# Kernel tuning notes

Hardware: AMD Instinct MI355X
Metric: run time of the kernel (lower is better)

Reference implementation:

```python
import jax, jax.numpy as jnp
import numpy as np

B = 256          # batch_size (number of graphs)
N = 512          # padded nodes per graph
IN_FEATS = 74
DIM = 128
E = 1_048_576    # total edges in batched graph
N_NODES = B * N


def setup_inputs() -> dict:
    key = jax.random.key(0)
    ks = jax.random.split(key, 10)
    x = jax.random.normal(ks[0], (N_NODES, IN_FEATS), dtype=jnp.float32)
    src = jax.random.randint(ks[1], (E,), 0, N_NODES, dtype=jnp.int32)
    dst = jax.random.randint(ks[2], (E,), 0, N_NODES, dtype=jnp.int32)
    # init_transform: Linear(in_feats, dim_embedding, bias=False); padding=True
    # zeroes weight[-1] (last OUTPUT row) -> last column in [in, out] layout.
    W_init = jax.random.normal(ks[3], (IN_FEATS, DIM), dtype=jnp.float32) * 0.1
    W_init = W_init.at[:, -1].set(0.0)
    W1 = jax.random.normal(ks[4], (DIM, DIM), dtype=jnp.float32) * 0.1
    W2 = jax.random.normal(ks[5], (DIM, DIM), dtype=jnp.float32) * 0.1
    W3 = jax.random.normal(ks[6], (DIM, DIM), dtype=jnp.float32) * 0.1
    b1 = jnp.zeros((DIM,), dtype=jnp.float32)
    b2 = jnp.zeros((DIM,), dtype=jnp.float32)
    b3 = jnp.zeros((DIM,), dtype=jnp.float32)
    return {"x": x, "src": src, "dst": dst, "W_init": W_init,
            "W1": W1, "b1": b1, "W2": W2, "b2": b2, "W3": W3, "b3": b3}


def _gcn_forward(x, src, dst, W_init, Ws, bs):
    n = x.shape[0]
    h = x @ W_init                                    # [n, DIM] initial embedding
    ones = jnp.ones(src.shape[0], dtype=x.dtype)
    deg_out = jax.ops.segment_sum(ones, src, num_segments=n)
    deg_in = jax.ops.segment_sum(ones, dst, num_segments=n)
    nrm_src = jax.lax.rsqrt(jnp.clip(deg_out, 1.0))   # D_out^{-1/2}
    nrm_dst = jax.lax.rsqrt(jnp.clip(deg_in, 1.0))    # D_in^{-1/2}
    for W, b in zip(Ws, bs):
        m = (h * nrm_src[:, None])[src]               # gather normalized messages [E, DIM]
        agg = jax.ops.segment_sum(m, dst, num_segments=n)  # scatter-add to dst nodes
        h = jax.nn.relu((agg * nrm_dst[:, None]) @ W + b)
    return h.reshape(B, N, -1)                        # [B, N, output_feats]


def reference(x, src, dst, W_init, W1, b1, W2, b2, W3, b3):
    return _gcn_forward(x, src, dst, W_init, (W1, W2, W3), (b1, b2, b3))
```

## Files before the change

kernel.cpp:

```cpp
#include <hip/hip_runtime.h>

#define NN 131072
#define NE 1048576
#define OFF_DEG_OUT 0x000000
#define OFF_CURSOR  0x080000
#define OFF_WT      0x100000
#define OFF_WTI     0x118000
#define OFF_BUCKET  0x200000
#define OFF_HN      0x2200000

typedef __attribute__((ext_vector_type(8))) short bf16x8;
typedef __attribute__((ext_vector_type(4))) float f32x4;

static __device__ __forceinline__ float blo(unsigned u){ return __uint_as_float(u << 16); }
static __device__ __forceinline__ float bhi(unsigned u){ return __uint_as_float(u & 0xffff0000u); }
static __device__ __forceinline__ unsigned f2b(float f){
    unsigned u = __float_as_uint(f);
    return (u + 0x7fffu + ((u >> 16) & 1u)) >> 16;
}
static __device__ __forceinline__ unsigned pack2(float a, float b){
    return f2b(a) | (f2b(b) << 16);
}

__global__ __launch_bounds__(256) void k_fill(const int* __restrict__ src,
                                              const int* __restrict__ dst,
                                              int* __restrict__ deg_out,
                                              int* __restrict__ cursor,
                                              int* __restrict__ bucket) {
    int base = (blockIdx.x * 256 + threadIdx.x) * 2;
    int2 s2 = *(const int2*)&src[base];
    int2 d2 = *(const int2*)&dst[base];
    int p0 = atomicAdd(&cursor[d2.x], 1);
    int p1 = atomicAdd(&cursor[d2.y], 1);
    atomicAdd(&deg_out[s2.x], 1);
    atomicAdd(&deg_out[s2.y], 1);
    if (p0 < 64) bucket[(size_t)d2.x * 64 + p0] = s2.x;
    if (p1 < 64) bucket[(size_t)d2.y * 64 + p1] = s2.y;
}

__global__ __launch_bounds__(256) void k_wprep(const float* __restrict__ W1,
                                               const float* __restrict__ W2,
                                               const float* __restrict__ W3,
                                               const float* __restrict__ Wi,
                                               unsigned short* __restrict__ Wt,
                                               unsigned short* __restrict__ Wti) {
    int idx = blockIdx.x * 256 + threadIdx.x;
    if (idx < 49152) {
        int L = idx >> 14, rem = idx & 16383;
        int k = rem >> 7, n = rem & 127;
        const float* W = L == 0 ? W1 : (L == 1 ? W2 : W3);
        Wt[L * 16384 + n * 128 + k] = (unsigned short)f2b(W[k * 128 + n]);
    } else if (idx < 61440) {
        int rem = idx - 49152;
        int n = rem / 96, k = rem - n * 96;
        float v = (k < 74) ? Wi[k * 128 + n] : 0.f;
        Wti[n * 96 + k] = (unsigned short)f2b(v);
    }
}

__global__ __launch_bounds__(256) void k_init(const float* __restrict__ X,
                                              const unsigned short* __restrict__ Wti,
                                              const int* __restrict__ deg_out,
                                              unsigned short* __restrict__ hn) {
    __shared__ unsigned int xs[64 * 68];
    int tid = threadIdx.x;
    int m0 = blockIdx.x * 64;

    for (int idx = tid; idx < 2368; idx += 256) {
        int m = idx / 37, t = idx - m * 37;
        float2 v = *(const float2*)&X[(size_t)(m0 + m) * 74 + t * 2];
        xs[m * 68 + t] = pack2(v.x, v.y);
    }
    for (int idx = tid; idx < 64 * 11; idx += 256) {
        int m = idx / 11, c = 37 + idx % 11;
        xs[m * 68 + c] = 0u;
    }
    __syncthreads();

    int wave = tid >> 6, lane = tid & 63, quad = lane >> 4, l16 = lane & 15;
    f32x4 acc[8];
    #pragma unroll
    for (int t = 0; t < 8; ++t) acc[t] = (f32x4){0.f, 0.f, 0.f, 0.f};
    int arow = (wave * 16 + l16) * 68 + quad * 4;
    #pragma unroll
    for (int ks = 0; ks < 3; ++ks) {
        bf16x8 af = *(const bf16x8*)&xs[arow + ks * 16];
        #pragma unroll
        for (int t = 0; t < 8; ++t) {
            bf16x8 bf = *(const bf16x8*)(Wti + (t * 16 + l16) * 96 + ks * 32 + quad * 8);
            acc[t] = __builtin_amdgcn_mfma_f32_16x16x32_bf16(af, bf, acc[t], 0, 0, 0);
        }
    }
    __syncthreads();
    unsigned short* atb = (unsigned short*)xs;
    int mb = wave * 16 + quad * 4;
    float nsr[4];
    #pragma unroll
    for (int r = 0; r < 4; ++r) {
        int dq = deg_out[m0 + mb + r];
        nsr[r] = rsqrtf((float)(dq > 1 ? dq : 1));
    }
    #pragma unroll
    for (int t = 0; t < 8; ++t)
        #pragma unroll
        for (int r = 0; r < 4; ++r)
            atb[(mb + r) * 136 + t * 16 + l16] = (unsigned short)f2b(acc[t][r] * nsr[r]);
    __syncthreads();
    {
        int r = tid >> 2, c0 = (tid & 3) * 32;
        unsigned int* sp = &xs[r * 68 + (tid & 3) * 16];
        #pragma unroll
        for (int j = 0; j < 4; ++j)
            *(uint4*)(hn + (size_t)(m0 + r) * 128 + c0 + j * 8) = *(const uint4*)(sp + j * 4);
    }
}

__global__ __launch_bounds__(256) void k_layer(const uint4* __restrict__ hn4,
                                               const int* __restrict__ bucket,
                                               const int* __restrict__ deg_in,
                                               const int* __restrict__ deg_out,
                                               const unsigned short* __restrict__ Wt,
                                               const float* __restrict__ bias,
                                               void* __restrict__ OutP, int last) {
    __shared__ unsigned int at[64 * 68];
    int tid = threadIdx.x;
    int m0 = blockIdx.x * 64;

    int g = tid >> 4, l16p = tid & 15;
    #pragma unroll
    for (int pass = 0; pass < 4; ++pass) {
        int nl = pass * 16 + g;
        int n = m0 + nl;
        int cnt = deg_in[n];
        cnt = cnt < 64 ? cnt : 64;
        const int* brow = bucket + (size_t)n * 64;
        float a0 = 0, a1 = 0, a2 = 0, a3 = 0, a4 = 0, a5 = 0, a6 = 0, a7 = 0;
        for (int c = 0; c < cnt; c += 8) {
            int4 sA = *(const int4*)&brow[c];
            int4 sB = *(const int4*)&brow[c + 4];
            int lim = cnt - c;
            int i1 = lim > 1 ? sA.y : 0;
            int i2 = lim > 2 ? sA.z : 0;
            int i3 = lim > 3 ? sA.w : 0;
            int i4 = lim > 4 ? sB.x : 0;
            int i5 = lim > 5 ? sB.y : 0;
            int i6 = lim > 6 ? sB.z : 0;
            int i7 = lim > 7 ? sB.w : 0;
            uint4 v0 = hn4[(size_t)sA.x * 16 + l16p];
            uint4 v1 = hn4[(size_t)i1 * 16 + l16p];
            uint4 v2 = hn4[(size_t)i2 * 16 + l16p];
            uint4 v3 = hn4[(size_t)i3 * 16 + l16p];
            uint4 v4 = hn4[(size_t)i4 * 16 + l16p];
            uint4 v5 = hn4[(size_t)i5 * 16 + l16p];
            uint4 v6 = hn4[(size_t)i6 * 16 + l16p];
            uint4 v7 = hn4[(size_t)i7 * 16 + l16p];
            float w1 = lim > 1 ? 1.f : 0.f;
            float w2 = lim > 2 ? 1.f : 0.f;
            float w3 = lim > 3 ? 1.f : 0.f;
            float w4 = lim > 4 ? 1.f : 0.f;
            float w5 = lim > 5 ? 1.f : 0.f;
            float w6 = lim > 6 ? 1.f : 0.f;
            float w7 = lim > 7 ? 1.f : 0.f;
            a0 += blo(v0.x); a1 += bhi(v0.x); a2 += blo(v0.y); a3 += bhi(v0.y);
            a4 += blo(v0.z); a5 += bhi(v0.z); a6 += blo(v0.w); a7 += bhi(v0.w);
            a0 = fmaf(w1, blo(v1.x), a0); a1 = fmaf(w1, bhi(v1.x), a1);
            a2 = fmaf(w1, blo(v1.y), a2); a3 = fmaf(w1, bhi(v1.y), a3);
            a4 = fmaf(w1, blo(v1.z), a4); a5 = fmaf(w1, bhi(v1.z), a5);
            a6 = fmaf(w1, blo(v1.w), a6); a7 = fmaf(w1, bhi(v1.w), a7);
            a0 = fmaf(w2, blo(v2.x), a0); a1 = fmaf(w2, bhi(v2.x), a1);
            a2 = fmaf(w2, blo(v2.y), a2); a3 = fmaf(w2, bhi(v2.y), a3);
            a4 = fmaf(w2, blo(v2.z), a4); a5 = fmaf(w2, bhi(v2.z), a5);
            a6 = fmaf(w2, blo(v2.w), a6); a7 = fmaf(w2, bhi(v2.w), a7);
            a0 = fmaf(w3, blo(v3.x), a0); a1 = fmaf(w3, bhi(v3.x), a1);
            a2 = fmaf(w3, blo(v3.y), a2); a3 = fmaf(w3, bhi(v3.y), a3);
            a4 = fmaf(w3, blo(v3.z), a4); a5 = fmaf(w3, bhi(v3.z), a5);
            a6 = fmaf(w3, blo(v3.w), a6); a7 = fmaf(w3, bhi(v3.w), a7);
            a0 = fmaf(w4, blo(v4.x), a0); a1 = fmaf(w4, bhi(v4.x), a1);
            a2 = fmaf(w4, blo(v4.y), a2); a3 = fmaf(w4, bhi(v4.y), a3);
            a4 = fmaf(w4, blo(v4.z), a4); a5 = fmaf(w4, bhi(v4.z), a5);
            a6 = fmaf(w4, blo(v4.w), a6); a7 = fmaf(w4, bhi(v4.w), a7);
            a0 = fmaf(w5, blo(v5.x), a0); a1 = fmaf(w5, bhi(v5.x), a1);
            a2 = fmaf(w5, blo(v5.y), a2); a3 = fmaf(w5, bhi(v5.y), a3);
            a4 = fmaf(w5, blo(v5.z), a4); a5 = fmaf(w5, bhi(v5.z), a5);
            a6 = fmaf(w5, blo(v5.w), a6); a7 = fmaf(w5, bhi(v5.w), a7);
            a0 = fmaf(w6, blo(v6.x), a0); a1 = fmaf(w6, bhi(v6.x), a1);
            a2 = fmaf(w6, blo(v6.y), a2); a3 = fmaf(w6, bhi(v6.y), a3);
            a4 = fmaf(w6, blo(v6.z), a4); a5 = fmaf(w6, bhi(v6.z), a5);
            a6 = fmaf(w6, blo(v6.w), a6); a7 = fmaf(w6, bhi(v6.w), a7);
            a0 = fmaf(w7, blo(v7.x), a0); a1 = fmaf(w7, bhi(v7.x), a1);
            a2 = fmaf(w7, blo(v7.y), a2); a3 = fmaf(w7, bhi(v7.y), a3);
            a4 = fmaf(w7, blo(v7.z), a4); a5 = fmaf(w7, bhi(v7.z), a5);
            a6 = fmaf(w7, blo(v7.w), a6); a7 = fmaf(w7, bhi(v7.w), a7);
        }
        float nd = rsqrtf((float)(cnt > 1 ? cnt : 1));
        uint4 o;
        o.x = pack2(a0 * nd, a1 * nd); o.y = pack2(a2 * nd, a3 * nd);
        o.z = pack2(a4 * nd, a5 * nd); o.w = pack2(a6 * nd, a7 * nd);
        *(uint4*)&at[nl * 68 + l16p * 4] = o;
    }
    __syncthreads();

    f32x4 acc[8];
    #pragma unroll
    for (int t = 0; t < 8; ++t) acc[t] = (f32x4){0.f, 0.f, 0.f, 0.f};
    int wave = tid >> 6, lane = tid & 63, quad = lane >> 4, l16 = lane & 15;
    int arow = (wave * 16 + l16) * 68 + quad * 4;
    #pragma unroll
    for (int ks = 0; ks < 4; ++ks) {
        bf16x8 af = *(const bf16x8*)&at[arow + ks * 16];
        #pragma unroll
        for (int t = 0; t < 8; ++t) {
            bf16x8 bf = *(const bf16x8*)(Wt + (t * 16 + l16) * 128 + ks * 32 + quad * 8);
            acc[t] = __builtin_amdgcn_mfma_f32_16x16x32_bf16(af, bf, acc[t], 0, 0, 0);
        }
    }

    int mb = wave * 16 + quad * 4;
    if (!last) {
        float nsr[4];
        #pragma unroll
        for (int r = 0; r < 4; ++r) {
            int dq = deg_out[m0 + mb + r];
            nsr[r] = rsqrtf((float)(dq > 1 ? dq : 1));
        }
        __syncthreads();
        unsigned short* atb = (unsigned short*)at;
        #pragma unroll
        for (int t = 0; t < 8; ++t) {
            float bv = bias[t * 16 + l16];
            #pragma unroll
            for (int r = 0; r < 4; ++r) {
                float v = acc[t][r] + bv;
                v = (v > 0.f ? v : 0.f) * nsr[r];
                atb[(mb + r) * 136 + t * 16 + l16] = (unsigned short)f2b(v);
            }
        }
        __syncthreads();
        int r = tid >> 2, c0 = (tid & 3) * 32;
        unsigned short* Out = (unsigned short*)OutP;
        unsigned int* sp = &at[r * 68 + (tid & 3) * 16];
        #pragma unroll
        for (int j = 0; j < 4; ++j)
            *(uint4*)(Out + (size_t)(m0 + r) * 128 + c0 + j * 8) = *(const uint4*)(sp + j * 4);
    } else {
        float* Out = (float*)OutP;
        #pragma unroll
        for (int t = 0; t < 8; ++t) {
            float bv = bias[t * 16 + l16];
            #pragma unroll
            for (int r = 0; r < 4; ++r) {
                float v = acc[t][r] + bv;
                v = v > 0.f ? v : 0.f;
                Out[(size_t)(m0 + mb + r) * 128 + t * 16 + l16] = v;
            }
        }
    }
}

extern "C" void kernel_launch(void* const* d_in, const int* in_sizes, int n_in,
                              void* d_out, int out_size, void* d_ws, size_t ws_size,
                              hipStream_t stream) {
    const float* x  = (const float*)d_in[0];
    const int* src  = (const int*)d_in[1];
    const int* dst  = (const int*)d_in[2];
    const float* Wi = (const float*)d_in[3];
    const float* W1 = (const float*)d_in[4];
    const float* b1 = (const float*)d_in[5];
    const float* W2 = (const float*)d_in[6];
    const float* b2 = (const float*)d_in[7];
    const float* W3 = (const float*)d_in[8];
    const float* b3 = (const float*)d_in[9];

    char* ws = (char*)d_ws;
    int* deg_out   = (int*)(ws + OFF_DEG_OUT);
    int* cursor    = (int*)(ws + OFF_CURSOR);
    unsigned short* Wt  = (unsigned short*)(ws + OFF_WT);
    unsigned short* Wti = (unsigned short*)(ws + OFF_WTI);
    int* bucket    = (int*)(ws + OFF_BUCKET);
    unsigned short* hnA = (unsigned short*)(ws + OFF_HN);
    unsigned short* hnB = (unsigned short*)d_out;

    hipMemsetAsync(ws, 0, 0x100000, stream);
    k_fill<<<NE / 512, 256, 0, stream>>>(src, dst, deg_out, cursor, bucket);
    k_wprep<<<240, 256, 0, stream>>>(W1, W2, W3, Wi, Wt, Wti);
    k_init<<<NN / 64, 256, 0, stream>>>(x, Wti, deg_out, hnA);

    const float* bl[3] = {b1, b2, b3};
    k_layer<<<NN / 64, 256, 0, stream>>>((const uint4*)hnA, bucket, cursor, deg_out,
                                         Wt,         bl[0], (void*)hnB, 0);
    k_layer<<<NN / 64, 256, 0, stream>>>((const uint4*)hnB, bucket, cursor, deg_out,
                                         Wt + 16384, bl[1], (void*)hnA, 0);
    k_layer<<<NN / 64, 256, 0, stream>>>((const uint4*)hnA, bucket, cursor, deg_out,
                                         Wt + 32768, bl[2], d_out, 1);
}
```

Before: 445.3 us.

## Gather neighbors with one wave per node and readlane-broadcast indices

Restructures the aggregation phase so each wave processes 16 destination nodes in turn. The 64 lanes each cover 2 bf16 features of a 128-wide row, and neighbor indices are loaded once per node and broadcast with readlane. This replaces the old scheme, where 16 lanes each did 16-byte loads of per-node index vectors. The aim is to make each gathered row load one contiguous wave-wide access and to cut per-thread register and index-load overhead. In exchange there are narrower 4-byte loads per lane and a serial loop over 16 nodes per wave. The final-layer output now uses nontemporal stores.

```diff
diff --git a/kernel.cpp b/kernel.cpp
--- a/kernel.cpp
+++ b/kernel.cpp
@@ -115,7 +115,7 @@
     }
 }
 
-__global__ __launch_bounds__(256) void k_layer(const uint4* __restrict__ hn4,
+__global__ __launch_bounds__(256) void k_layer(const unsigned short* __restrict__ hn,
                                                const int* __restrict__ bucket,
                                                const int* __restrict__ deg_in,
                                                const int* __restrict__ deg_out,
@@ -124,86 +124,41 @@
                                                void* __restrict__ OutP, int last) {
     __shared__ unsigned int at[64 * 68];
     int tid = threadIdx.x;
+    int wave = tid >> 6, lane = tid & 63;
     int m0 = blockIdx.x * 64;
 
-    int g = tid >> 4, l16p = tid & 15;
-    #pragma unroll
-    for (int pass = 0; pass < 4; ++pass) {
-        int nl = pass * 16 + g;
+    for (int i = 0; i < 16; ++i) {
+        int nl = wave * 16 + i;
         int n = m0 + nl;
         int cnt = deg_in[n];
         cnt = cnt < 64 ? cnt : 64;
-        const int* brow = bucket + (size_t)n * 64;
-        float a0 = 0, a1 = 0, a2 = 0, a3 = 0, a4 = 0, a5 = 0, a6 = 0, a7 = 0;
+        int myidx = bucket[(size_t)n * 64 + lane];
+        float a0 = 0.f, a1 = 0.f;
         for (int c = 0; c < cnt; c += 8) {
-            int4 sA = *(const int4*)&brow[c];
-            int4 sB = *(const int4*)&brow[c + 4];
-            int lim = cnt - c;
-            int i1 = lim > 1 ? sA.y : 0;
-            int i2 = lim > 2 ? sA.z : 0;
-            int i3 = lim > 3 ? sA.w : 0;
-            int i4 = lim > 4 ? sB.x : 0;
-            int i5 = lim > 5 ? sB.y : 0;
-            int i6 = lim > 6 ? sB.z : 0;
-            int i7 = lim > 7 ? sB.w : 0;
-            uint4 v0 = hn4[(size_t)sA.x * 16 + l16p];
-            uint4 v1 = hn4[(size_t)i1 * 16 + l16p];
-            uint4 v2 = hn4[(size_t)i2 * 16 + l16p];
-            uint4 v3 = hn4[(size_t)i3 * 16 + l16p];
-            uint4 v4 = hn4[(size_t)i4 * 16 + l16p];
-            uint4 v5 = hn4[(size_t)i5 * 16 + l16p];
-            uint4 v6 = hn4[(size_t)i6 * 16 + l16p];
-            uint4 v7 = hn4[(size_t)i7 * 16 + l16p];
-            float w1 = lim > 1 ? 1.f : 0.f;
-            float w2 = lim > 2 ? 1.f : 0.f;
-            float w3 = lim > 3 ? 1.f : 0.f;
-            float w4 = lim > 4 ? 1.f : 0.f;
-            float w5 = lim > 5 ? 1.f : 0.f;
-            float w6 = lim > 6 ? 1.f : 0.f;
-            float w7 = lim > 7 ? 1.f : 0.f;
-            a0 += blo(v0.x); a1 += bhi(v0.x); a2 += blo(v0.y); a3 += bhi(v0.y);
-            a4 += blo(v0.z); a5 += bhi(v0.z); a6 += blo(v0.w); a7 += bhi(v0.w);
-            a0 = fmaf(w1, blo(v1.x), a0); a1 = fmaf(w1, bhi(v1.x), a1);
-            a2 = fmaf(w1, blo(v1.y), a2); a3 = fmaf(w1, bhi(v1.y), a3);
-            a4 = fmaf(w1, blo(v1.z), a4); a5 = fmaf(w1, bhi(v1.z), a5);
-            a6 = fmaf(w1, blo(v1.w), a6); a7 = fmaf(w1, bhi(v1.w), a7);
-            a0 = fmaf(w2, blo(v2.x), a0); a1 = fmaf(w2, bhi(v2.x), a1);
-            a2 = fmaf(w2, blo(v2.y), a2); a3 = fmaf(w2, bhi(v2.y), a3);
-            a4 = fmaf(w2, blo(v2.z), a4); a5 = fmaf(w2, bhi(v2.z), a5);
-            a6 = fmaf(w2, blo(v2.w), a6); a7 = fmaf(w2, bhi(v2.w), a7);
-            a0 = fmaf(w3, blo(v3.x), a0); a1 = fmaf(w3, bhi(v3.x), a1);
-            a2 = fmaf(w3, blo(v3.y), a2); a3 = fmaf(w3, bhi(v3.y), a3);
-            a4 = fmaf(w3, blo(v3.z), a4); a5 = fmaf(w3, bhi(v3.z), a5);
-            a6 = fmaf(w3, blo(v3.w), a6); a7 = fmaf(w3, bhi(v3.w), a7);
-            a0 = fmaf(w4, blo(v4.x), a0); a1 = fmaf(w4, bhi(v4.x), a1);
-            a2 = fmaf(w4, blo(v4.y), a2); a3 = fmaf(w4, bhi(v4.y), a3);
-            a4 = fmaf(w4, blo(v4.z), a4); a5 = fmaf(w4, bhi(v4.z), a5);
-            a6 = fmaf(w4, blo(v4.w), a6); a7 = fmaf(w4, bhi(v4.w), a7);
-            a0 = fmaf(w5, blo(v5.x), a0); a1 = fmaf(w5, bhi(v5.x), a1);
-            a2 = fmaf(w5, blo(v5.y), a2); a3 = fmaf(w5, bhi(v5.y), a3);
-            a4 = fmaf(w5, blo(v5.z), a4); a5 = fmaf(w5, bhi(v5.z), a5);
-            a6 = fmaf(w5, blo(v5.w), a6); a7 = fmaf(w5, bhi(v5.w), a7);
-            a0 = fmaf(w6, blo(v6.x), a0); a1 = fmaf(w6, bhi(v6.x), a1);
-            a2 = fmaf(w6, blo(v6.y), a2); a3 = fmaf(w6, bhi(v6.y), a3);
-            a4 = fmaf(w6, blo(v6.z), a4); a5 = fmaf(w6, bhi(v6.z), a5);
-            a6 = fmaf(w6, blo(v6.w), a6); a7 = fmaf(w6, bhi(v6.w), a7);
-            a0 = fmaf(w7, blo(v7.x), a0); a1 = fmaf(w7, bhi(v7.x), a1);
-            a2 = fmaf(w7, blo(v7.y), a2); a3 = fmaf(w7, bhi(v7.y), a3);
-            a4 = fmaf(w7, blo(v7.z), a4); a5 = fmaf(w7, bhi(v7.z), a5);
-            a6 = fmaf(w7, blo(v7.w), a6); a7 = fmaf(w7, bhi(v7.w), a7);
+            unsigned v[8];
+            float w[8];
+            #pragma unroll
+            for (int j = 0; j < 8; ++j) {
+                int jj = c + j;
+                int s = jj < cnt ? __builtin_amdgcn_readlane(myidx, jj) : 0;
+                w[j] = jj < cnt ? 1.f : 0.f;
+                v[j] = *(const unsigned*)(hn + (size_t)s * 128 + lane * 2);
+            }
+            #pragma unroll
+            for (int j = 0; j < 8; ++j) {
+                a0 = fmaf(w[j], blo(v[j]), a0);
+                a1 = fmaf(w[j], bhi(v[j]), a1);
+            }
         }
         float nd = rsqrtf((float)(cnt > 1 ? cnt : 1));
-        uint4 o;
-        o.x = pack2(a0 * nd, a1 * nd); o.y = pack2(a2 * nd, a3 * nd);
-        o.z = pack2(a4 * nd, a5 * nd); o.w = pack2(a6 * nd, a7 * nd);
-        *(uint4*)&at[nl * 68 + l16p * 4] = o;
+        at[nl * 68 + lane] = pack2(a0 * nd, a1 * nd);
     }
     __syncthreads();
 
     f32x4 acc[8];
     #pragma unroll
     for (int t = 0; t < 8; ++t) acc[t] = (f32x4){0.f, 0.f, 0.f, 0.f};
-    int wave = tid >> 6, lane = tid & 63, quad = lane >> 4, l16 = lane & 15;
+    int quad = lane >> 4, l16 = lane & 15;
     int arow = (wave * 16 + l16) * 68 + quad * 4;
     #pragma unroll
     for (int ks = 0; ks < 4; ++ks) {
@@ -251,7 +206,7 @@
             for (int r = 0; r < 4; ++r) {
                 float v = acc[t][r] + bv;
                 v = v > 0.f ? v : 0.f;
-                Out[(size_t)(m0 + mb + r) * 128 + t * 16 + l16] = v;
+                __builtin_nontemporal_store(v, &Out[(size_t)(m0 + mb + r) * 128 + t * 16 + l16]);
             }
         }
     }
@@ -286,10 +241,10 @@
     k_init<<<NN / 64, 256, 0, stream>>>(x, Wti, deg_out, hnA);
 
     const float* bl[3] = {b1, b2, b3};
-    k_layer<<<NN / 64, 256, 0, stream>>>((const uint4*)hnA, bucket, cursor, deg_out,
+    k_layer<<<NN / 64, 256, 0, stream>>>(hnA, bucket, cursor, deg_out,
                                          Wt,         bl[0], (void*)hnB, 0);
-    k_layer<<<NN / 64, 256, 0, stream>>>((const uint4*)hnB, bucket, cursor, deg_out,
+    k_layer<<<NN / 64, 256, 0, stream>>>(hnB, bucket, cursor, deg_out,
                                          Wt + 16384, bl[1], (void*)hnA, 0);
-    k_layer<<<NN / 64, 256, 0, stream>>>((const uint4*)hnA, bucket, cursor, deg_out,
+    k_layer<<<NN / 64, 256, 0, stream>>>(hnA, bucket, cursor, deg_out,
                                          Wt + 32768, bl[2], d_out, 1);
 }
```

Result: slower. 502.1 us (+12.8%).
